# Performance work log

Measured on AMD Instinct MI355X. Metric: run time of the kernel, lower is better.

The kernel has to match this reference:

```python
import jax, jax.numpy as jnp
import numpy as np
from jax import lax

KR = 2                      # kernel_radius
KS = 2 * KR + 1             # kernel_size = 5
ITER = 3                    # iter_time
THETA = jnp.float32(np.pi * 0.5)


def _sobel_kernels():
    # window_size=3, mult=2 -> classic Sobel (cross-correlation form)
    mx = np.zeros((3, 3), np.float32)
    my = np.zeros((3, 3), np.float32)
    for j in range(-1, 2):
        for i in range(-1, 2):
            d = float(i * i + j * j)
            if d != 0:
                mx[j + 1, i + 1] = 2.0 * i / d
                my[j + 1, i + 1] = 2.0 * j / d
    return jnp.asarray(mx), jnp.asarray(my)


def _grouped_conv(x, k2d):
    # x: (B,C,H,W); per-channel 3x3 cross-correlation, zero padding 1 (F.conv2d semantics)
    C = x.shape[1]
    kern = jnp.broadcast_to(k2d[None, None], (C, 1, 3, 3))
    return lax.conv_general_dilated(
        x, kern, window_strides=(1, 1), padding=[(1, 1), (1, 1)],
        feature_group_count=C, dimension_numbers=("NCHW", "OIHW", "NCHW"))


def _reflect_pad(x, r):
    return jnp.pad(x, ((0, 0), (0, 0), (r, r), (r, r)), mode="reflect")


def _patches(xpad, h, w):
    # xpad: (B,C,h+2r,w+2r) -> (B,C,h,w,KS,KS); static slices, KS*KS=25 views
    rows = []
    for i in range(KS):
        cols = [xpad[:, :, i:i + h, j:j + w] for j in range(KS)]
        rows.append(jnp.stack(cols, axis=-1))
    return jnp.stack(rows, axis=-2)  # (B,C,h,w,i,j)


def reference(img):
    B, C, h, w = img.shape
    img_n = img / jnp.amax(img, axis=(2, 3), keepdims=True)

    sx, sy = _sobel_kernels()
    gx = _grouped_conv(img_n, sx)
    gy = _grouped_conv(img_n, sy)
    # torch.clamp(min=1e-12): negatives are clipped up (faithful to source)
    gx = jnp.maximum(gx, 1e-12)
    gy = jnp.maximum(gy, 1e-12)

    gmag = jnp.sqrt(gx * gx + gy * gy)
    gnorm = gmag / jnp.amax(gmag, axis=(2, 3), keepdims=True)
    xn = gx / gmag
    yn = gy / gmag
    ct, st = jnp.cos(THETA), jnp.sin(THETA)  # fp32 rotation by pi/2
    xn, yn = xn * ct - yn * st, yn * ct + xn * st

    # Wm: 0.5*(1+tanh(eta*(neighbor_gradnorm - center_gradnorm))); Ws == 1
    g_nb = _patches(_reflect_pad(gnorm, KR), h, w)          # (B,C,h,w,k,k)
    Wm = 0.5 * (1.0 + jnp.tanh(g_nb - gnorm[..., None, None]))

    for _ in range(ITER):
        # Wd*phi == X.Y (abs * sign recombines exactly, incl. 0)
        Yx = _patches(_reflect_pad(xn, KR), h, w)
        Yy = _patches(_reflect_pad(yn, KR), h, w)
        dot = xn[..., None, None] * Yx + yn[..., None, None] * Yy
        kernels = Wm * dot                                   # phi*Ws*Wm*Wd

        mx = _patches(_reflect_pad(gnorm * xn, KR), h, w)
        my = _patches(_reflect_pad(gnorm * yn, KR), h, w)
        xr = jnp.sum(mx * kernels, axis=(-2, -1))
        yr = jnp.sum(my * kernels, axis=(-2, -1))
        mag = jnp.sqrt(xr * xr + yr * yr)
        xn = xr / mag
        yn = yr / mag

    angle = jnp.arctan(-yn / xn)
    a = 180.0 * angle / jnp.float32(np.pi)
    # F.instance_norm: per-(B,C) spatial standardization, biased var, eps=1e-5
    mean = jnp.mean(a, axis=(2, 3), keepdims=True)
    var = jnp.var(a, axis=(2, 3), keepdims=True)
    return (a - mean) / jnp.sqrt(var + 1e-5)


def setup_inputs() -> dict:
    key = jax.random.key(0)
    img = jax.random.uniform(key, (2, 3, 512, 512), dtype=jnp.float32)
    return {"img": img}
```

## Files before the change

### kernel.cpp

```cpp
#include <hip/hip_runtime.h>
#include <math.h>

#define H 512
#define W 512
#define HW (H * W)
#define NCH 6

__device__ __forceinline__ int reflect_idx(int p, int n) {
    if (p < 0) p = -p;
    if (p >= n) p = 2 * n - 2 - p;
    return p;
}

__global__ __launch_bounds__(256) void k_sobel(const float* __restrict__ img,
                                               float* __restrict__ gpart,
                                               float* __restrict__ g,
                                               float* __restrict__ xn,
                                               float* __restrict__ yn) {
    const int SW = 132;
    __shared__ float st[10 * SW];

    int ch = blockIdx.z;
    int bx0 = blockIdx.x * 128, by0 = blockIdx.y * 8;
    int tx = threadIdx.x, ty = threadIdx.y;
    int tid = ty * 32 + tx;
    const float* im = img + (size_t)ch * HW;

#pragma unroll
    for (int jr = 0; jr < 2; ++jr) {
        int r = ty + 8 * jr;
        if (jr == 0 || ty < 2) {
            int yy = by0 - 1 + r;
            bool yok = (yy >= 0 && yy < H);
            const float* rowp = im + yy * W;
#pragma unroll
            for (int m = 0; m < 4; ++m) {
                int c = tx + 32 * m;
                int xx = bx0 - 1 + c;
                float v = 0.f;
                if (yok && xx >= 0 && xx < W) v = rowp[xx];
                st[r * SW + c] = v;
            }
            if (tx < 2) {
                int c = 128 + tx;
                int xx = bx0 - 1 + c;
                float v = 0.f;
                if (yok && xx >= 0 && xx < W) v = rowp[xx];
                st[r * SW + c] = v;
            }
        }
    }
    __syncthreads();

    float bmax = 0.f;
    int y = by0 + ty;
    int r = ty + 1;
    float gm4[4], xr4[4], yr4[4];
#pragma unroll
    for (int k = 0; k < 4; ++k) {
        int c = tx + 32 * k + 1;
        float a00 = st[(r - 1) * SW + c - 1], a01 = st[(r - 1) * SW + c], a02 = st[(r - 1) * SW + c + 1];
        float a10 = st[r * SW + c - 1], a12 = st[r * SW + c + 1];
        float a20 = st[(r + 1) * SW + c - 1], a21 = st[(r + 1) * SW + c], a22 = st[(r + 1) * SW + c + 1];

        float gx = (a02 - a00) + 2.f * (a12 - a10) + (a22 - a20);
        float gy = (a20 - a00) + 2.f * (a21 - a01) + (a22 - a02);

        gx = fmaxf(gx, 1e-12f);
        gy = fmaxf(gy, 1e-12f);
        float d = gx * gx + gy * gy;
        float rq = __builtin_amdgcn_rsqf(d);
        float gm = d * rq;
        float xv = gx * rq, yv = gy * rq;
        const float ct = -4.37113883e-08f;
        gm4[k] = gm;
        xr4[k] = xv * ct - yv;
        yr4[k] = yv * ct + xv;
        bmax = fmaxf(bmax, gm);
    }
#pragma unroll
    for (int k = 0; k < 4; ++k) {
        int idx = y * W + bx0 + tx + 32 * k;
        float* gc = g + (size_t)ch * HW;
        float* xc = xn + (size_t)ch * HW;
        float* yc = yn + (size_t)ch * HW;
        gc[idx] = gm4[k];
        xc[idx] = xr4[k];
        yc[idx] = yr4[k];
    }

    __syncthreads();
    st[tid] = bmax;
    __syncthreads();
    for (int s = 128; s > 0; s >>= 1) {
        if (tid < s) st[tid] = fmaxf(st[tid], st[tid + s]);
        __syncthreads();
    }
    if (tid == 0) gpart[ch * 256 + blockIdx.y * 4 + blockIdx.x] = st[0];
}

__global__ __launch_bounds__(64) void k_red(const float* __restrict__ gpart,
                                            float* __restrict__ gmax) {
    int ch = blockIdx.x;
    int t = threadIdx.x;
    const float* gp = gpart + ch * 256;
    float m = fmaxf(fmaxf(gp[t], gp[t + 64]), fmaxf(gp[t + 128], gp[t + 192]));
#pragma unroll
    for (int k = 32; k > 0; k >>= 1) m = fmaxf(m, __shfl_xor(m, k, 64));
    if (t == 0) gmax[ch] = m;
}

struct W8 { float w[8]; };

template <bool LAST>
__global__ __launch_bounds__(256) void k_iter(const float* __restrict__ g,
                                              const float* __restrict__ xin,
                                              const float* __restrict__ yin,
                                              const float* __restrict__ gmaxp,
                                              float* __restrict__ xout,
                                              float* __restrict__ yout,
                                              double* __restrict__ partials) {
    const int SW = 136;
    __shared__ __align__(16) float sg[12 * SW];
    __shared__ __align__(16) float se[12 * SW];
    __shared__ __align__(16) float sx[12 * SW];
    __shared__ __align__(16) float sy[12 * SW];
    __shared__ double swr[8];

    int ch = blockIdx.z;
    int bx0 = blockIdx.x * 128, by0 = blockIdx.y * 8;
    int tx = threadIdx.x, ty = threadIdx.y;
    int tid = ty * 32 + tx;
    const size_t cbase = (size_t)ch * HW;

    float s2 = -2.f * __builtin_amdgcn_rcpf(gmaxp[ch]);

    const float* gc = g + cbase;
    const float* xc = xin + cbase;
    const float* yc = yin + cbase;
#pragma unroll
    for (int jr = 0; jr < 2; ++jr) {
        int r = ty + 8 * jr;
        if (jr == 0 || ty < 4) {
            int yy = reflect_idx(by0 - 2 + r, H);
            const float* grow = gc + yy * W;
            const float* xrow = xc + yy * W;
            const float* yrow = yc + yy * W;
#pragma unroll
            for (int m = 0; m < 5; ++m) {
                int c = (m < 4) ? (tx + 32 * m) : (128 + tx);
                if (m < 4 || tx < 4) {
                    int xx = reflect_idx(bx0 - 2 + c, W);
                    int s = r * SW + c;
                    float gv = grow[xx];
                    sg[s] = gv;
                    se[s] = __expf(s2 * gv);
                    sx[s] = xrow[xx];
                    sy[s] = yrow[xx];
                }
            }
        }
    }
    __syncthreads();

    auto LD8 = [&](const float* s, int r) {
        W8 o;
        const float4* p = (const float4*)(s + r * SW + 4 * tx);
        float4 a = p[0], b = p[1];
        o.w[0] = a.x; o.w[1] = a.y; o.w[2] = a.z; o.w[3] = a.w;
        o.w[4] = b.x; o.w[5] = b.y; o.w[6] = b.z; o.w[7] = b.w;
        return o;
    };

    int row0 = ty + 2;
    W8 cxw = LD8(sx, row0), cyw = LD8(sy, row0), cew = LD8(se, row0);
    float cx[4], cy[4], ec[4];
#pragma unroll
    for (int k = 0; k < 4; ++k) {
        cx[k] = cxw.w[k + 2];
        cy[k] = cyw.w[k + 2];
        ec[k] = __builtin_amdgcn_rcpf(cew.w[k + 2]);
    }

    float xr[4] = {0.f, 0.f, 0.f, 0.f}, yr[4] = {0.f, 0.f, 0.f, 0.f};
#pragma unroll
    for (int dy = -2; dy <= 2; ++dy) {
        W8 gw = LD8(sg, row0 + dy), xw = LD8(sx, row0 + dy),
           yw = LD8(sy, row0 + dy), ew = LD8(se, row0 + dy);
#pragma unroll
        for (int k = 0; k < 4; ++k) {
#pragma unroll
            for (int dxi = 0; dxi < 5; ++dxi) {
                int n = k + dxi;
                float dot = cx[k] * xw.w[n] + cy[k] * yw.w[n];
                float wm = __builtin_amdgcn_rcpf(1.f + ew.w[n] * ec[k]);
                float m = gw.w[n] * (wm * dot);
                xr[k] = fmaf(m, xw.w[n], xr[k]);
                yr[k] = fmaf(m, yw.w[n], yr[k]);
            }
        }
    }

    size_t obase = cbase + (size_t)(by0 + ty) * W + bx0 + 4 * tx;
    if (!LAST) {
        float ox[4], oy[4];
#pragma unroll
        for (int k = 0; k < 4; ++k) {
            float im2 = __builtin_amdgcn_rsqf(xr[k] * xr[k] + yr[k] * yr[k]);
            ox[k] = xr[k] * im2;
            oy[k] = yr[k] * im2;
        }
        *(float4*)(xout + obase) = make_float4(ox[0], ox[1], ox[2], ox[3]);
        *(float4*)(yout + obase) = make_float4(oy[0], oy[1], oy[2], oy[3]);
    } else {
        float a[4];
        double s = 0.0, q = 0.0;
#pragma unroll
        for (int k = 0; k < 4; ++k) {
            float ang = atanf(-yr[k] / xr[k]);
            a[k] = (180.f * ang) / 3.14159274f;
            s += (double)a[k];
            q += (double)a[k] * (double)a[k];
        }
        *(float4*)(xout + obase) = make_float4(a[0], a[1], a[2], a[3]);

#pragma unroll
        for (int off = 32; off > 0; off >>= 1) {
            s += __shfl_down(s, off, 64);
            q += __shfl_down(q, off, 64);
        }
        if ((tid & 63) == 0) {
            swr[tid >> 6] = s;
            swr[4 + (tid >> 6)] = q;
        }
        __syncthreads();
        if (tid == 0) {
            double ts = swr[0] + swr[1] + swr[2] + swr[3];
            double tq = swr[4] + swr[5] + swr[6] + swr[7];
            int blk = blockIdx.y * 4 + blockIdx.x;
            partials[((size_t)ch * 256 + blk) * 2 + 0] = ts;
            partials[((size_t)ch * 256 + blk) * 2 + 1] = tq;
        }
    }
}

__global__ __launch_bounds__(256) void k_norm(float* __restrict__ a,
                                              const double* __restrict__ partials) {
    int ch = blockIdx.y;
    int t = threadIdx.x;

    __shared__ double rs[256], rq[256];
    rs[t] = partials[((size_t)ch * 256 + t) * 2 + 0];
    rq[t] = partials[((size_t)ch * 256 + t) * 2 + 1];
    __syncthreads();
    for (int st = 128; st > 0; st >>= 1) {
        if (t < st) {
            rs[t] += rs[t + st];
            rq[t] += rq[t + st];
        }
        __syncthreads();
    }
    __shared__ float sm, ss;
    if (t == 0) {
        double mean = rs[0] / (double)HW;
        double var = rq[0] / (double)HW - mean * mean;
        sm = (float)mean;
        ss = (float)(1.0 / sqrt(var + 1e-5));
    }
    __syncthreads();
    float mean = sm, sc = ss;

    float4* a4 = (float4*)(a + (size_t)ch * HW + (size_t)blockIdx.x * 4096);
#pragma unroll
    for (int k = 0; k < 4; ++k) {
        float4 v = a4[k * 256 + t];
        v.x = (v.x - mean) * sc;
        v.y = (v.y - mean) * sc;
        v.z = (v.z - mean) * sc;
        v.w = (v.w - mean) * sc;
        a4[k * 256 + t] = v;
    }
}

extern "C" void kernel_launch(void* const* d_in, const int* in_sizes, int n_in,
                              void* d_out, int out_size, void* d_ws, size_t ws_size,
                              hipStream_t stream) {
    (void)in_sizes; (void)n_in; (void)out_size; (void)ws_size;
    const float* img = (const float*)d_in[0];
    float* out = (float*)d_out;

    float* wsf = (float*)d_ws;
    float* gmax = wsf + 8;
    float* gpart = wsf + 512;
    double* partials = (double*)(wsf + 8192);
    float* g = wsf + 32768;
    float* xnA = g + (size_t)NCH * HW;
    float* ynA = xnA + (size_t)NCH * HW;
    float* xnB = ynA + (size_t)NCH * HW;
    float* ynB = xnB + (size_t)NCH * HW;

    dim3 tile_grid(4, 64, NCH), tile_blk(32, 8);

    k_sobel<<<tile_grid, tile_blk, 0, stream>>>(img, gpart, g, xnA, ynA);
    k_red<<<dim3(NCH), dim3(64), 0, stream>>>(gpart, gmax);
    k_iter<false><<<tile_grid, tile_blk, 0, stream>>>(g, xnA, ynA, gmax, xnB, ynB, nullptr);
    k_iter<false><<<tile_grid, tile_blk, 0, stream>>>(g, xnB, ynB, gmax, xnA, ynA, nullptr);
    k_iter<true><<<tile_grid, tile_blk, 0, stream>>>(g, xnA, ynA, gmax, out, nullptr, partials);
    k_norm<<<dim3(64, NCH), dim3(256), 0, stream>>>(out, partials);
}
```

Measured before the change: 124.6 us.

## Fuse two ETF iterations per tile with halo recompute and inline gmax reduction

Merges the first two refinement iterations into one kernel that loads a 4-pixel halo, computes iteration 1 over a 12-row by 132-column region into shared memory, then computes iteration 2 from it. The separate gmax reduction kernel is removed and each block reduces the Sobel partial maxima itself with a wave shuffle. This drops one global round trip of the x/y fields and two kernel launches. In exchange it recomputes the overlapping halo (about 50% extra work in the fused kernel), uses more shared memory per block and does some unaligned wide LDS reads.

```diff
diff --git a/kernel.cpp b/kernel.cpp
--- a/kernel.cpp
+++ b/kernel.cpp
@@ -17,8 +17,8 @@
                                                float* __restrict__ g,
                                                float* __restrict__ xn,
                                                float* __restrict__ yn) {
-    const int SW = 132;
-    __shared__ float st[10 * SW];
+    const int SB = 132;
+    __shared__ float st[10 * SB];
 
     int ch = blockIdx.z;
     int bx0 = blockIdx.x * 128, by0 = blockIdx.y * 8;
@@ -39,14 +39,14 @@
                 int xx = bx0 - 1 + c;
                 float v = 0.f;
                 if (yok && xx >= 0 && xx < W) v = rowp[xx];
-                st[r * SW + c] = v;
+                st[r * SB + c] = v;
             }
             if (tx < 2) {
                 int c = 128 + tx;
                 int xx = bx0 - 1 + c;
                 float v = 0.f;
                 if (yok && xx >= 0 && xx < W) v = rowp[xx];
-                st[r * SW + c] = v;
+                st[r * SB + c] = v;
             }
         }
     }
@@ -59,9 +59,9 @@
 #pragma unroll
     for (int k = 0; k < 4; ++k) {
         int c = tx + 32 * k + 1;
-        float a00 = st[(r - 1) * SW + c - 1], a01 = st[(r - 1) * SW + c], a02 = st[(r - 1) * SW + c + 1];
-        float a10 = st[r * SW + c - 1], a12 = st[r * SW + c + 1];
-        float a20 = st[(r + 1) * SW + c - 1], a21 = st[(r + 1) * SW + c], a22 = st[(r + 1) * SW + c + 1];
+        float a00 = st[(r - 1) * SB + c - 1], a01 = st[(r - 1) * SB + c], a02 = st[(r - 1) * SB + c + 1];
+        float a10 = st[r * SB + c - 1], a12 = st[r * SB + c + 1];
+        float a20 = st[(r + 1) * SB + c - 1], a21 = st[(r + 1) * SB + c], a22 = st[(r + 1) * SB + c + 1];
 
         float gx = (a02 - a00) + 2.f * (a12 - a10) + (a22 - a20);
         float gy = (a20 - a00) + 2.f * (a21 - a01) + (a22 - a02);
@@ -99,33 +99,90 @@
     if (tid == 0) gpart[ch * 256 + blockIdx.y * 4 + blockIdx.x] = st[0];
 }
 
-__global__ __launch_bounds__(64) void k_red(const float* __restrict__ gpart,
-                                            float* __restrict__ gmax) {
-    int ch = blockIdx.x;
-    int t = threadIdx.x;
+#define SWI 136
+
+struct W8 { float w[8]; };
+
+__device__ __forceinline__ W8 ld8(const float* p) {
+    W8 o;
+    const float4* q = (const float4*)p;
+    float4 a = q[0], b = q[1];
+    o.w[0] = a.x; o.w[1] = a.y; o.w[2] = a.z; o.w[3] = a.w;
+    o.w[4] = b.x; o.w[5] = b.y; o.w[6] = b.z; o.w[7] = b.w;
+    return o;
+}
+
+__device__ __forceinline__ W8 ld12w(const float* p) {
+    W8 o;
+    const float4* q = (const float4*)p;
+    float4 a = q[0], b = q[1], c = q[2];
+    o.w[0] = a.z; o.w[1] = a.w; o.w[2] = b.x; o.w[3] = b.y;
+    o.w[4] = b.z; o.w[5] = b.w; o.w[6] = c.x; o.w[7] = c.y;
+    return o;
+}
+
+__device__ __forceinline__ void contrib8(const W8& gw, const W8& xw, const W8& yw, const W8& ew,
+                                         const float* cx, const float* cy, const float* ec,
+                                         float* xr, float* yr) {
+#pragma unroll
+    for (int k = 0; k < 4; ++k) {
+#pragma unroll
+        for (int d = 0; d < 5; ++d) {
+            int n = k + d;
+            float dot = cx[k] * xw.w[n] + cy[k] * yw.w[n];
+            float wm = __builtin_amdgcn_rcpf(1.f + ew.w[n] * ec[k]);
+            float m = gw.w[n] * (wm * dot);
+            xr[k] = fmaf(m, xw.w[n], xr[k]);
+            yr[k] = fmaf(m, yw.w[n], yr[k]);
+        }
+    }
+}
+
+template <int WIDE>
+__device__ __forceinline__ void etf_group(const float* sg, const float* se,
+                                          const float* sx, const float* sy,
+                                          int base, float* xr, float* yr) {
+    W8 cxw = WIDE ? ld12w(sx + base) : ld8(sx + base);
+    W8 cyw = WIDE ? ld12w(sy + base) : ld8(sy + base);
+    W8 cew = WIDE ? ld12w(se + base) : ld8(se + base);
+    float cx[4], cy[4], ec[4];
+#pragma unroll
+    for (int k = 0; k < 4; ++k) {
+        cx[k] = cxw.w[k + 2];
+        cy[k] = cyw.w[k + 2];
+        ec[k] = __builtin_amdgcn_rcpf(cew.w[k + 2]);
+    }
+#pragma unroll
+    for (int k = 0; k < 4; ++k) { xr[k] = 0.f; yr[k] = 0.f; }
+#pragma unroll
+    for (int dy = -2; dy <= 2; ++dy) {
+        int rb = base + dy * SWI;
+        W8 gw = WIDE ? ld12w(sg + rb) : ld8(sg + rb);
+        W8 xw = WIDE ? ld12w(sx + rb) : ld8(sx + rb);
+        W8 yw = WIDE ? ld12w(sy + rb) : ld8(sy + rb);
+        W8 ew = WIDE ? ld12w(se + rb) : ld8(se + rb);
+        contrib8(gw, xw, yw, ew, cx, cy, ec, xr, yr);
+    }
+}
+
+__device__ __forceinline__ float wave_gmax_s2(const float* gpart, int ch, int lane) {
     const float* gp = gpart + ch * 256;
-    float m = fmaxf(fmaxf(gp[t], gp[t + 64]), fmaxf(gp[t + 128], gp[t + 192]));
+    float m = fmaxf(fmaxf(gp[lane], gp[lane + 64]), fmaxf(gp[lane + 128], gp[lane + 192]));
 #pragma unroll
     for (int k = 32; k > 0; k >>= 1) m = fmaxf(m, __shfl_xor(m, k, 64));
-    if (t == 0) gmax[ch] = m;
-}
-
-struct W8 { float w[8]; };
-
-template <bool LAST>
-__global__ __launch_bounds__(256) void k_iter(const float* __restrict__ g,
-                                              const float* __restrict__ xin,
-                                              const float* __restrict__ yin,
-                                              const float* __restrict__ gmaxp,
-                                              float* __restrict__ xout,
-                                              float* __restrict__ yout,
-                                              double* __restrict__ partials) {
-    const int SW = 136;
-    __shared__ __align__(16) float sg[12 * SW];
-    __shared__ __align__(16) float se[12 * SW];
-    __shared__ __align__(16) float sx[12 * SW];
-    __shared__ __align__(16) float sy[12 * SW];
-    __shared__ double swr[8];
+    return -2.f * __builtin_amdgcn_rcpf(m);
+}
+
+__global__ __launch_bounds__(256) void k_iterA(const float* __restrict__ g,
+                                               const float* __restrict__ xin,
+                                               const float* __restrict__ yin,
+                                               const float* __restrict__ gpart,
+                                               float* __restrict__ xout,
+                                               float* __restrict__ yout) {
+    __shared__ __align__(16) float sg[16 * SWI];
+    __shared__ __align__(16) float se[16 * SWI];
+    __shared__ __align__(16) float sx[16 * SWI];
+    __shared__ __align__(16) float sy[16 * SWI];
 
     int ch = blockIdx.z;
     int bx0 = blockIdx.x * 128, by0 = blockIdx.y * 8;
@@ -133,7 +190,106 @@
     int tid = ty * 32 + tx;
     const size_t cbase = (size_t)ch * HW;
 
-    float s2 = -2.f * __builtin_amdgcn_rcpf(gmaxp[ch]);
+    float s2 = wave_gmax_s2(gpart, ch, tid & 63);
+
+    const float* gc = g + cbase;
+    const float* xc = xin + cbase;
+    const float* yc = yin + cbase;
+#pragma unroll
+    for (int jr = 0; jr < 2; ++jr) {
+        int r = ty + 8 * jr;
+        {
+            int yy = reflect_idx(by0 - 4 + r, H);
+            const float* grow = gc + yy * W;
+            const float* xrow = xc + yy * W;
+            const float* yrow = yc + yy * W;
+#pragma unroll
+            for (int m = 0; m < 5; ++m) {
+                int c = (m < 4) ? (tx + 32 * m) : (128 + tx);
+                if (m < 4 || tx < 8) {
+                    int xx = reflect_idx(bx0 - 4 + c, W);
+                    int s = r * SWI + c;
+                    float gv = grow[xx];
+                    sg[s] = gv;
+                    se[s] = __expf(s2 * gv);
+                    sx[s] = xrow[xx];
+                    sy[s] = yrow[xx];
+                }
+            }
+        }
+    }
+    __syncthreads();
+
+    float oax[2][4], oay[2][4];
+#pragma unroll
+    for (int rnd = 0; rnd < 2; ++rnd) {
+        int gi = tid + rnd * 256;
+        if (rnd == 0 || gi < 396) {
+            int gr = gi / 33, gm = gi - gr * 33;
+            int base = (2 + gr) * SWI + 4 * gm;
+            float xr[4], yr[4];
+            etf_group<0>(sg, se, sx, sy, base, xr, yr);
+#pragma unroll
+            for (int k = 0; k < 4; ++k) {
+                float iv = __builtin_amdgcn_rsqf(xr[k] * xr[k] + yr[k] * yr[k]);
+                oax[rnd][k] = xr[k] * iv;
+                oay[rnd][k] = yr[k] * iv;
+            }
+        }
+    }
+    __syncthreads();
+#pragma unroll
+    for (int rnd = 0; rnd < 2; ++rnd) {
+        int gi = tid + rnd * 256;
+        if (rnd == 0 || gi < 396) {
+            int gr = gi / 33, gm = gi - gr * 33;
+            int c0 = (2 + gr) * SWI + 2 + 4 * gm;
+            *(float2*)&sx[c0] = make_float2(oax[rnd][0], oax[rnd][1]);
+            *(float2*)&sx[c0 + 2] = make_float2(oax[rnd][2], oax[rnd][3]);
+            *(float2*)&sy[c0] = make_float2(oay[rnd][0], oay[rnd][1]);
+            *(float2*)&sy[c0 + 2] = make_float2(oay[rnd][2], oay[rnd][3]);
+        }
+    }
+    __syncthreads();
+
+    {
+        int gm = tid & 31, gr = tid >> 5;
+        int base = (4 + gr) * SWI + 4 * gm;
+        float xr[4], yr[4];
+        etf_group<1>(sg, se, sx, sy, base, xr, yr);
+
+        float ox[4], oy[4];
+#pragma unroll
+        for (int k = 0; k < 4; ++k) {
+            float iv = __builtin_amdgcn_rsqf(xr[k] * xr[k] + yr[k] * yr[k]);
+            ox[k] = xr[k] * iv;
+            oy[k] = yr[k] * iv;
+        }
+        size_t obase = cbase + (size_t)(by0 + gr) * W + bx0 + 4 * gm;
+        *(float4*)(xout + obase) = make_float4(ox[0], ox[1], ox[2], ox[3]);
+        *(float4*)(yout + obase) = make_float4(oy[0], oy[1], oy[2], oy[3]);
+    }
+}
+
+__global__ __launch_bounds__(256) void k_iterB(const float* __restrict__ g,
+                                               const float* __restrict__ xin,
+                                               const float* __restrict__ yin,
+                                               const float* __restrict__ gpart,
+                                               float* __restrict__ out,
+                                               double* __restrict__ partials) {
+    __shared__ __align__(16) float sg[12 * SWI];
+    __shared__ __align__(16) float se[12 * SWI];
+    __shared__ __align__(16) float sx[12 * SWI];
+    __shared__ __align__(16) float sy[12 * SWI];
+    __shared__ double swr[8];
+
+    int ch = blockIdx.z;
+    int bx0 = blockIdx.x * 128, by0 = blockIdx.y * 8;
+    int tx = threadIdx.x, ty = threadIdx.y;
+    int tid = ty * 32 + tx;
+    const size_t cbase = (size_t)ch * HW;
+
+    float s2 = wave_gmax_s2(gpart, ch, tid & 63);
 
     const float* gc = g + cbase;
     const float* xc = xin + cbase;
@@ -151,7 +307,7 @@
                 int c = (m < 4) ? (tx + 32 * m) : (128 + tx);
                 if (m < 4 || tx < 4) {
                     int xx = reflect_idx(bx0 - 2 + c, W);
-                    int s = r * SW + c;
+                    int s = r * SWI + c;
                     float gv = grow[xx];
                     sg[s] = gv;
                     se[s] = __expf(s2 * gv);
@@ -163,58 +319,12 @@
     }
     __syncthreads();
 
-    auto LD8 = [&](const float* s, int r) {
-        W8 o;
-        const float4* p = (const float4*)(s + r * SW + 4 * tx);
-        float4 a = p[0], b = p[1];
-        o.w[0] = a.x; o.w[1] = a.y; o.w[2] = a.z; o.w[3] = a.w;
-        o.w[4] = b.x; o.w[5] = b.y; o.w[6] = b.z; o.w[7] = b.w;
-        return o;
-    };
-
-    int row0 = ty + 2;
-    W8 cxw = LD8(sx, row0), cyw = LD8(sy, row0), cew = LD8(se, row0);
-    float cx[4], cy[4], ec[4];
-#pragma unroll
-    for (int k = 0; k < 4; ++k) {
-        cx[k] = cxw.w[k + 2];
-        cy[k] = cyw.w[k + 2];
-        ec[k] = __builtin_amdgcn_rcpf(cew.w[k + 2]);
-    }
-
-    float xr[4] = {0.f, 0.f, 0.f, 0.f}, yr[4] = {0.f, 0.f, 0.f, 0.f};
-#pragma unroll
-    for (int dy = -2; dy <= 2; ++dy) {
-        W8 gw = LD8(sg, row0 + dy), xw = LD8(sx, row0 + dy),
-           yw = LD8(sy, row0 + dy), ew = LD8(se, row0 + dy);
-#pragma unroll
-        for (int k = 0; k < 4; ++k) {
-#pragma unroll
-            for (int dxi = 0; dxi < 5; ++dxi) {
-                int n = k + dxi;
-                float dot = cx[k] * xw.w[n] + cy[k] * yw.w[n];
-                float wm = __builtin_amdgcn_rcpf(1.f + ew.w[n] * ec[k]);
-                float m = gw.w[n] * (wm * dot);
-                xr[k] = fmaf(m, xw.w[n], xr[k]);
-                yr[k] = fmaf(m, yw.w[n], yr[k]);
-            }
-        }
-    }
-
-    size_t obase = cbase + (size_t)(by0 + ty) * W + bx0 + 4 * tx;
-    if (!LAST) {
-        float ox[4], oy[4];
-#pragma unroll
-        for (int k = 0; k < 4; ++k) {
-            float im2 = __builtin_amdgcn_rsqf(xr[k] * xr[k] + yr[k] * yr[k]);
-            ox[k] = xr[k] * im2;
-            oy[k] = yr[k] * im2;
-        }
-        *(float4*)(xout + obase) = make_float4(ox[0], ox[1], ox[2], ox[3]);
-        *(float4*)(yout + obase) = make_float4(oy[0], oy[1], oy[2], oy[3]);
-    } else {
-        float a[4];
-        double s = 0.0, q = 0.0;
+    float a[4];
+    double s = 0.0, q = 0.0;
+    {
+        int base = (ty + 2) * SWI + 4 * tx;
+        float xr[4], yr[4];
+        etf_group<0>(sg, se, sx, sy, base, xr, yr);
 #pragma unroll
         for (int k = 0; k < 4; ++k) {
             float ang = atanf(-yr[k] / xr[k]);
@@ -222,25 +332,26 @@
             s += (double)a[k];
             q += (double)a[k] * (double)a[k];
         }
-        *(float4*)(xout + obase) = make_float4(a[0], a[1], a[2], a[3]);
-
-#pragma unroll
-        for (int off = 32; off > 0; off >>= 1) {
-            s += __shfl_down(s, off, 64);
-            q += __shfl_down(q, off, 64);
-        }
-        if ((tid & 63) == 0) {
-            swr[tid >> 6] = s;
-            swr[4 + (tid >> 6)] = q;
-        }
-        __syncthreads();
-        if (tid == 0) {
-            double ts = swr[0] + swr[1] + swr[2] + swr[3];
-            double tq = swr[4] + swr[5] + swr[6] + swr[7];
-            int blk = blockIdx.y * 4 + blockIdx.x;
-            partials[((size_t)ch * 256 + blk) * 2 + 0] = ts;
-            partials[((size_t)ch * 256 + blk) * 2 + 1] = tq;
-        }
+        size_t obase = cbase + (size_t)(by0 + ty) * W + bx0 + 4 * tx;
+        *(float4*)(out + obase) = make_float4(a[0], a[1], a[2], a[3]);
+    }
+
+#pragma unroll
+    for (int off = 32; off > 0; off >>= 1) {
+        s += __shfl_down(s, off, 64);
+        q += __shfl_down(q, off, 64);
+    }
+    if ((tid & 63) == 0) {
+        swr[tid >> 6] = s;
+        swr[4 + (tid >> 6)] = q;
+    }
+    __syncthreads();
+    if (tid == 0) {
+        double ts = swr[0] + swr[1] + swr[2] + swr[3];
+        double tq = swr[4] + swr[5] + swr[6] + swr[7];
+        int blk = blockIdx.y * 4 + blockIdx.x;
+        partials[((size_t)ch * 256 + blk) * 2 + 0] = ts;
+        partials[((size_t)ch * 256 + blk) * 2 + 1] = tq;
     }
 }
 
@@ -290,7 +401,6 @@
     float* out = (float*)d_out;
 
     float* wsf = (float*)d_ws;
-    float* gmax = wsf + 8;
     float* gpart = wsf + 512;
     double* partials = (double*)(wsf + 8192);
     float* g = wsf + 32768;
@@ -302,9 +412,7 @@
     dim3 tile_grid(4, 64, NCH), tile_blk(32, 8);
 
     k_sobel<<<tile_grid, tile_blk, 0, stream>>>(img, gpart, g, xnA, ynA);
-    k_red<<<dim3(NCH), dim3(64), 0, stream>>>(gpart, gmax);
-    k_iter<false><<<tile_grid, tile_blk, 0, stream>>>(g, xnA, ynA, gmax, xnB, ynB, nullptr);
-    k_iter<false><<<tile_grid, tile_blk, 0, stream>>>(g, xnB, ynB, gmax, xnA, ynA, nullptr);
-    k_iter<true><<<tile_grid, tile_blk, 0, stream>>>(g, xnA, ynA, gmax, out, nullptr, partials);
+    k_iterA<<<tile_grid, tile_blk, 0, stream>>>(g, xnA, ynA, gpart, xnB, ynB);
+    k_iterB<<<tile_grid, tile_blk, 0, stream>>>(g, xnB, ynB, gpart, out, partials);
     k_norm<<<dim3(64, NCH), dim3(256), 0, stream>>>(out, partials);
 }
```

Measured after the change: 149.1 us. +19.6%, slower.
